# Kernel tuning notes

Hardware: AMD Instinct MI355X
Metric: run time of the kernel (lower is better)

The kernel has to match this reference:

```python
import jax, jax.numpy as jnp
import numpy as np
from jax import lax

# dims: S=seq_len, B=batch, D=word dim, HE=encoder hidden, HD=decoder hidden,
# E=atomic embedding dim, A=num_atomic, T=max_steps, SOS=start token id
S, B, D = 48, 64, 300
HE, HD, E, A, T, SOS = 300, 256, 50, 128, 50, 1


def _u(key, shape, scale):
    return jax.random.uniform(key, shape, jnp.float32, -scale, scale)


def setup_inputs() -> dict:
    key = jax.random.key(0)
    ks = iter(jax.random.split(key, 64))
    inp = {"word_vectors": jax.random.normal(next(ks), (S, B, D), jnp.float32)}
    se = 1.0 / np.sqrt(HE)
    for l, din in ((0, D), (1, 2 * HE)):
        for d in ("f", "b"):
            inp[f"e{l}{d}_Wih"] = _u(next(ks), (3 * HE, din), se)
            inp[f"e{l}{d}_Whh"] = _u(next(ks), (3 * HE, HE), se)
            inp[f"e{l}{d}_bih"] = _u(next(ks), (3 * HE,), se)
            inp[f"e{l}{d}_bhh"] = _u(next(ks), (3 * HE,), se)
    sd = 1.0 / np.sqrt(HD)
    for l, din in ((0, E), (1, HD)):
        inp[f"d{l}_Wih"] = _u(next(ks), (3 * HD, din), sd)
        inp[f"d{l}_Whh"] = _u(next(ks), (3 * HD, HD), sd)
        inp[f"d{l}_bih"] = _u(next(ks), (3 * HD,), sd)
        inp[f"d{l}_bhh"] = _u(next(ks), (3 * HD,), sd)
    emb = jax.random.normal(next(ks), (A, E), jnp.float32)
    inp["emb"] = emb.at[0].set(0.0)  # padding_idx=0
    inp["Wout"] = _u(next(ks), (A, HD), sd)
    inp["bout"] = _u(next(ks), (A,), sd)
    so = 1.0 / np.sqrt(D)
    inp["Wh0"] = _u(next(ks), (2 * HD, D), so)
    inp["bh0"] = _u(next(ks), (2 * HD,), so)
    return inp


def gru_cell(x, h, Wih, Whh, bih, bhh):
    # PyTorch GRU cell semantics
    gi = x @ Wih.T + bih
    gh = h @ Whh.T + bhh
    ir, iz, inn = jnp.split(gi, 3, axis=-1)
    hr, hz, hn = jnp.split(gh, 3, axis=-1)
    r = jax.nn.sigmoid(ir + hr)
    z = jax.nn.sigmoid(iz + hz)
    n = jnp.tanh(inn + r * hn)
    return (1.0 - z) * n + z * h


def gru_layer(xs, Wih, Whh, bih, bhh, reverse=False):
    # xs: [S, B, din] -> [S, B, H]; h0 = zeros (torch default)
    h0 = jnp.zeros((xs.shape[1], Whh.shape[1]), xs.dtype)
    def step(h, x):
        hn = gru_cell(x, h, Wih, Whh, bih, bhh)
        return hn, hn
    _, ys = lax.scan(step, h0, xs, reverse=reverse)
    return ys


def reference(word_vectors, e0f_Wih, e0f_Whh, e0f_bih, e0f_bhh, e0b_Wih, e0b_Whh, e0b_bih, e0b_bhh, e1f_Wih, e1f_Whh, e1f_bih, e1f_bhh, e1b_Wih, e1b_Whh, e1b_bih, e1b_bhh, d0_Wih, d0_Whh, d0_bih, d0_bhh, d1_Wih, d1_Whh, d1_bih, d1_bhh, emb, Wout, bout, Wh0, bh0):
    # --- encoder: 2-layer bidirectional GRU (eval mode: no dropout) ---
    x0f = gru_layer(word_vectors, e0f_Wih, e0f_Whh, e0f_bih, e0f_bhh, reverse=False)
    x0b = gru_layer(word_vectors, e0b_Wih, e0b_Whh, e0b_bih, e0b_bhh, reverse=True)
    x0 = jnp.concatenate([x0f, x0b], axis=-1)  # [S,B,2*HE]
    x1f = gru_layer(x0, e1f_Wih, e1f_Whh, e1f_bih, e1f_bhh, reverse=False)
    x1b = gru_layer(x0, e1b_Wih, e1b_Whh, e1b_bih, e1b_bhh, reverse=True)
    enc = x1f + x1b  # view(S,B,2,HE).sum(dim=2) of concat == sum of directions

    N = S * B
    h = jnp.tanh(enc @ Wh0.T + bh0).reshape(N, 2, HD)  # [N,2,HD]
    h0, h1 = h[:, 0], h[:, 1]
    e = jnp.broadcast_to(emb[SOS], (N, E))

    def step(carry, _):
        h0, h1, e = carry
        h0n = gru_cell(e, h0, d0_Wih, d0_Whh, d0_bih, d0_bhh)
        h1n = gru_cell(h0n, h1, d1_Wih, d1_Whh, d1_bih, d1_bhh)
        y = jax.nn.log_softmax(h1n @ Wout.T + bout, axis=-1)  # [N,A]
        p = jnp.argmax(y, axis=-1)
        return (h0n, h1n, emb[p]), y

    _, Y = lax.scan(step, (h0, h1, e), None, length=T)  # [T,N,A]
    return Y.reshape(T, S, B, A)[:-1]
```

## Files before the change

### kernel.cpp

```cpp
#include <hip/hip_runtime.h>
#include <math.h>

#define S_ 48
#define B_ 64
#define D_ 300
#define HE_ 300
#define HD_ 256
#define E_ 50
#define A_ 128
#define T_ 50
#define N_ (S_*B_)

__device__ __forceinline__ float sigm(float x){ return 1.0f/(1.0f + expf(-x)); }

template<int MODE>
__global__ __launch_bounds__(256)
void gemm_bias_kernel(const float* __restrict__ A, const float* __restrict__ A2,
                      const float* __restrict__ W,
                      const float* __restrict__ bias, float* __restrict__ C,
                      float* __restrict__ C2, int M, int N, int K)
{
  __shared__ float As[16][64];
  __shared__ float Ws[16][64];
  const int tid = threadIdx.x;
  const int bm = blockIdx.y * 64;
  const int bn = blockIdx.x * 64;
  const int tx = tid & 15, ty = tid >> 4;
  const int lr = tid >> 2;
  const int lk = (tid & 3) << 2;
  float acc[4][4] = {{0.f}};
  for (int kb = 0; kb < K; kb += 16) {
    {
      const int row = bm + lr;
      const int k = kb + lk;
      const float* ap = A + (size_t)row * K + k;
      float4 v = make_float4(0.f,0.f,0.f,0.f);
      if (k + 3 < K) v = *reinterpret_cast<const float4*>(ap);
      else {
        if (k   < K) v.x = ap[0];
        if (k+1 < K) v.y = ap[1];
        if (k+2 < K) v.z = ap[2];
        if (k+3 < K) v.w = ap[3];
      }
      if (MODE == 2) {
        const float* ap2 = A2 + (size_t)row * K + k;
        if (k + 3 < K) {
          float4 v2 = *reinterpret_cast<const float4*>(ap2);
          v.x += v2.x; v.y += v2.y; v.z += v2.z; v.w += v2.w;
        } else {
          if (k   < K) v.x += ap2[0];
          if (k+1 < K) v.y += ap2[1];
          if (k+2 < K) v.z += ap2[2];
          if (k+3 < K) v.w += ap2[3];
        }
      }
      As[lk][lr]=v.x; As[lk+1][lr]=v.y; As[lk+2][lr]=v.z; As[lk+3][lr]=v.w;
    }
    {
      const int col = bn + lr;
      const int k = kb + lk;
      float4 v = make_float4(0.f,0.f,0.f,0.f);
      if (col < N) {
        const float* wp = W + (size_t)col * K + k;
        if (k + 3 < K) v = *reinterpret_cast<const float4*>(wp);
        else {
          if (k   < K) v.x = wp[0];
          if (k+1 < K) v.y = wp[1];
          if (k+2 < K) v.z = wp[2];
          if (k+3 < K) v.w = wp[3];
        }
      }
      Ws[lk][lr]=v.x; Ws[lk+1][lr]=v.y; Ws[lk+2][lr]=v.z; Ws[lk+3][lr]=v.w;
    }
    __syncthreads();
    #pragma unroll
    for (int kk = 0; kk < 16; ++kk) {
      float4 a4 = *reinterpret_cast<const float4*>(&As[kk][ty<<2]);
      float4 w4 = *reinterpret_cast<const float4*>(&Ws[kk][tx<<2]);
      const float* a = reinterpret_cast<const float*>(&a4);
      const float* w = reinterpret_cast<const float*>(&w4);
      #pragma unroll
      for (int i = 0; i < 4; ++i)
        #pragma unroll
        for (int j = 0; j < 4; ++j)
          acc[i][j] = fmaf(a[i], w[j], acc[i][j]);
    }
    __syncthreads();
  }
  #pragma unroll
  for (int i = 0; i < 4; ++i) {
    const int m = bm + (ty<<2) + i;
    #pragma unroll
    for (int j = 0; j < 4; ++j) {
      const int n = bn + (tx<<2) + j;
      if (n < N) {
        float v = acc[i][j] + bias[n];
        if (MODE == 0) {
          C[(size_t)m*N + n] = v;
        } else {
          v = tanhf(v);
          if (n < HD_) C[(size_t)m*HD_ + n] = v;
          else         C2[(size_t)m*HD_ + (n-HD_)] = v;
        }
      }
    }
  }
}

__global__ __launch_bounds__(256)
void ctranspose_kernel(const float* __restrict__ in, float* __restrict__ out,
                       int NC, int NK, int NKP, int dstride, int row0, int coff)
{
  int idx = blockIdx.x * 256 + threadIdx.x;
  if (idx < NC*NKP) {
    int gc = idx / NKP, k = idx % NKP;
    out[(size_t)(row0+k)*dstride + coff + gc] =
        (k < NK) ? in[(size_t)gc*NK + k] : 0.0f;
  }
}

__global__ __launch_bounds__(256)
void pack4_kernel(const float* __restrict__ W, float4* __restrict__ P,
                  int NC, int NK, int K4)
{
  int idx = blockIdx.x * 256 + threadIdx.x;
  if (idx >= NC * K4) return;
  int k4 = idx / NC, gc = idx % NC;
  int k = k4 << 2;
  const float* wp = W + (size_t)gc * NK + k;
  float4 v = make_float4(0.f,0.f,0.f,0.f);
  if (k   < NK) v.x = wp[0];
  if (k+1 < NK) v.y = wp[1];
  if (k+2 < NK) v.z = wp[2];
  if (k+3 < NK) v.w = wp[3];
  P[(size_t)k4 * NC + gc] = v;
}

template<int LAYER>
__global__ __launch_bounds__(640, 2)
void enc_layer_persistent(const float* __restrict__ gi_f, const float* __restrict__ gi_b,
                          const float* __restrict__ WhhT_f, const float* __restrict__ WhhT_b,
                          const float* __restrict__ bhh_f, const float* __restrict__ bhh_b,
                          float* __restrict__ out, float* __restrict__ outB)
{
  const int dir = blockIdx.y;
  const float* gi  = dir ? gi_b   : gi_f;
  const float* WT  = dir ? WhhT_b : WhhT_f;
  const float* bhh = dir ? bhh_b  : bhh_f;
  float* o = (LAYER == 1 && dir) ? outB : out;

  __shared__ float hA[4][304];
  __shared__ float hB[4][304];
  const int tid = threadIdx.x;
  const int half = tid / 320;
  const int j = tid - half*320;
  const int R0 = blockIdx.x * 4;
  const int r0 = half * 2;
  const bool act = (j < HE_);

  float b_r = 0.f, b_z = 0.f, b_n = 0.f;
  if (act) { b_r = bhh[j]; b_z = bhh[HE_+j]; b_n = bhh[2*HE_+j]; }
  __syncthreads();

  for (int t = 0; t < S_; ++t) {
    const int tt = dir ? (S_-1 - t) : t;
    float (*hin)[304]  = (t & 1) ? hB : hA;
    float (*hout)[304] = (t & 1) ? hA : hB;
    float ar[2]={0,0}, az[2]={0,0}, an[2]={0,0};
    if (act && t > 0) {
      for (int k = 0; k < HE_; k += 4) {
        float wr[4], wz[4], wn[4];
        #pragma unroll
        for (int u = 0; u < 4; ++u) {
          const float* wk = WT + (size_t)(k+u)*(3*HE_);
          wr[u] = wk[j]; wz[u] = wk[HE_+j]; wn[u] = wk[2*HE_+j];
        }
        #pragma unroll
        for (int r = 0; r < 2; ++r) {
          float4 h4 = *reinterpret_cast<const float4*>(&hin[r0+r][k]);
          ar[r]=fmaf(h4.x,wr[0],ar[r]); ar[r]=fmaf(h4.y,wr[1],ar[r]);
          ar[r]=fmaf(h4.z,wr[2],ar[r]); ar[r]=fmaf(h4.w,wr[3],ar[r]);
          az[r]=fmaf(h4.x,wz[0],az[r]); az[r]=fmaf(h4.y,wz[1],az[r]);
          az[r]=fmaf(h4.z,wz[2],az[r]); az[r]=fmaf(h4.w,wz[3],az[r]);
          an[r]=fmaf(h4.x,wn[0],an[r]); an[r]=fmaf(h4.y,wn[1],an[r]);
          an[r]=fmaf(h4.z,wn[2],an[r]); an[r]=fmaf(h4.w,wn[3],an[r]);
        }
      }
    }
    if (act) {
      #pragma unroll
      for (int r = 0; r < 2; ++r) {
        const int row = R0 + r0 + r;
        const size_t gb = (size_t)(tt*B_ + row) * (3*HE_);
        float gr = gi[gb + j];
        float gz = gi[gb + HE_ + j];
        float gn = gi[gb + 2*HE_ + j];
        float rg = sigm(gr + ar[r] + b_r);
        float zg = sigm(gz + az[r] + b_z);
        float ng = tanhf(gn + rg*(an[r] + b_n));
        float ho = (t > 0) ? hin[r0+r][j] : 0.0f;
        float hn = (1.0f - zg)*ng + zg*ho;
        hout[r0+r][j] = hn;
        if (LAYER == 0) o[(size_t)(tt*B_ + row)*(2*HE_) + dir*HE_ + j] = hn;
        else            o[(size_t)(tt*B_ + row)*HE_ + j] = hn;
      }
    }
    __syncthreads();
  }
}

__global__ __launch_bounds__(512, 2)
void dec_persistent(const float4* __restrict__ Wih0P,
                    const float4* __restrict__ Whh0P,
                    const float4* __restrict__ Wih1P,
                    const float4* __restrict__ Whh1P,
                    const float* __restrict__ WoutT,
                    const float* __restrict__ bih0, const float* __restrict__ bhh0,
                    const float* __restrict__ bih1, const float* __restrict__ bhh1,
                    const float* __restrict__ bout,
                    const float* __restrict__ emb,
                    const float* __restrict__ h0init, const float* __restrict__ h1init,
                    float* __restrict__ Y)
{
  __shared__ __align__(16) float h0s[12][256];
  __shared__ __align__(16) float h1s[12][256];
  __shared__ __align__(16) float es[12][52];
  const int tid = threadIdx.x;
  const int R0 = blockIdx.x * 12;
  const int c  = tid & 255;
  const int half = tid >> 8;
  const int r0 = half * 6;
  const int lane = tid & 63;
  const int wave = tid >> 6;

  for (int i = tid; i < 12*64; i += 512) {
    int r = i >> 6, k = (i & 63) << 2;
    *reinterpret_cast<float4*>(&h0s[r][k]) =
        *reinterpret_cast<const float4*>(&h0init[(size_t)(R0+r)*HD_ + k]);
    *reinterpret_cast<float4*>(&h1s[r][k]) =
        *reinterpret_cast<const float4*>(&h1init[(size_t)(R0+r)*HD_ + k]);
  }
  for (int i = tid; i < 12*52; i += 512) {
    int r = i / 52, k = i - r*52;
    es[r][k] = (k < E_) ? emb[E_ + k] : 0.0f;
  }
  const float b0r = bih0[c] + bhh0[c];
  const float b0z = bih0[HD_+c] + bhh0[HD_+c];
  const float b0ni = bih0[2*HD_+c];
  const float b0nh = bhh0[2*HD_+c];
  const float b1r = bih1[c] + bhh1[c];
  const float b1z = bih1[HD_+c] + bhh1[HD_+c];
  const float b1ni = bih1[2*HD_+c];
  const float b1nh = bhh1[2*HD_+c];
  const float bo0 = bout[lane];
  const float bo1 = bout[64 + lane];
  __syncthreads();

  for (int s = 0; s < T_-1; ++s) {
    float ar[6]={0,0,0,0,0,0}, az[6]={0,0,0,0,0,0};
    float ani[6]={0,0,0,0,0,0}, anh[6]={0,0,0,0,0,0};
    for (int kq = 0; kq < 64; ++kq) {
      const int k = kq << 2;
      float4 wr = Whh0P[kq*768 + c];
      float4 wz = Whh0P[kq*768 + 256 + c];
      float4 wn = Whh0P[kq*768 + 512 + c];
      #pragma unroll
      for (int r = 0; r < 6; ++r) {
        float4 x = *reinterpret_cast<const float4*>(&h0s[r0+r][k]);
        ar[r]=fmaf(x.x,wr.x,ar[r]); ar[r]=fmaf(x.y,wr.y,ar[r]);
        ar[r]=fmaf(x.z,wr.z,ar[r]); ar[r]=fmaf(x.w,wr.w,ar[r]);
        az[r]=fmaf(x.x,wz.x,az[r]); az[r]=fmaf(x.y,wz.y,az[r]);
        az[r]=fmaf(x.z,wz.z,az[r]); az[r]=fmaf(x.w,wz.w,az[r]);
        anh[r]=fmaf(x.x,wn.x,anh[r]); anh[r]=fmaf(x.y,wn.y,anh[r]);
        anh[r]=fmaf(x.z,wn.z,anh[r]); anh[r]=fmaf(x.w,wn.w,anh[r]);
      }
      if (kq < 13) {
        float4 vr = Wih0P[kq*768 + c];
        float4 vz = Wih0P[kq*768 + 256 + c];
        float4 vn = Wih0P[kq*768 + 512 + c];
        #pragma unroll
        for (int r = 0; r < 6; ++r) {
          float4 e = *reinterpret_cast<const float4*>(&es[r0+r][k]);
          ar[r]=fmaf(e.x,vr.x,ar[r]); ar[r]=fmaf(e.y,vr.y,ar[r]);
          ar[r]=fmaf(e.z,vr.z,ar[r]); ar[r]=fmaf(e.w,vr.w,ar[r]);
          az[r]=fmaf(e.x,vz.x,az[r]); az[r]=fmaf(e.y,vz.y,az[r]);
          az[r]=fmaf(e.z,vz.z,az[r]); az[r]=fmaf(e.w,vz.w,az[r]);
          ani[r]=fmaf(e.x,vn.x,ani[r]); ani[r]=fmaf(e.y,vn.y,ani[r]);
          ani[r]=fmaf(e.z,vn.z,ani[r]); ani[r]=fmaf(e.w,vn.w,ani[r]);
        }
      }
    }
    __syncthreads();
    {
      float hnew[6];
      #pragma unroll
      for (int r = 0; r < 6; ++r) {
        float rg = sigm(ar[r] + b0r);
        float zg = sigm(az[r] + b0z);
        float ng = tanhf(ani[r] + b0ni + rg*(anh[r] + b0nh));
        float hold = h0s[r0+r][c];
        hnew[r] = (1.0f - zg)*ng + zg*hold;
      }
      #pragma unroll
      for (int r = 0; r < 6; ++r) h0s[r0+r][c] = hnew[r];
    }
    __syncthreads();
    #pragma unroll
    for (int r = 0; r < 6; ++r) { ar[r]=0.f; az[r]=0.f; ani[r]=0.f; anh[r]=0.f; }
    for (int kq = 0; kq < 64; ++kq) {
      const int k = kq << 2;
      float4 vr = Wih1P[kq*768 + c];
      float4 vz = Wih1P[kq*768 + 256 + c];
      float4 vn = Wih1P[kq*768 + 512 + c];
      float4 wr = Whh1P[kq*768 + c];
      float4 wz = Whh1P[kq*768 + 256 + c];
      float4 wn = Whh1P[kq*768 + 512 + c];
      #pragma unroll
      for (int r = 0; r < 6; ++r) {
        float4 x = *reinterpret_cast<const float4*>(&h0s[r0+r][k]);
        ar[r]=fmaf(x.x,vr.x,ar[r]); ar[r]=fmaf(x.y,vr.y,ar[r]);
        ar[r]=fmaf(x.z,vr.z,ar[r]); ar[r]=fmaf(x.w,vr.w,ar[r]);
        az[r]=fmaf(x.x,vz.x,az[r]); az[r]=fmaf(x.y,vz.y,az[r]);
        az[r]=fmaf(x.z,vz.z,az[r]); az[r]=fmaf(x.w,vz.w,az[r]);
        ani[r]=fmaf(x.x,vn.x,ani[r]); ani[r]=fmaf(x.y,vn.y,ani[r]);
        ani[r]=fmaf(x.z,vn.z,ani[r]); ani[r]=fmaf(x.w,vn.w,ani[r]);
        float4 y = *reinterpret_cast<const float4*>(&h1s[r0+r][k]);
        ar[r]=fmaf(y.x,wr.x,ar[r]); ar[r]=fmaf(y.y,wr.y,ar[r]);
        ar[r]=fmaf(y.z,wr.z,ar[r]); ar[r]=fmaf(y.w,wr.w,ar[r]);
        az[r]=fmaf(y.x,wz.x,az[r]); az[r]=fmaf(y.y,wz.y,az[r]);
        az[r]=fmaf(y.z,wz.z,az[r]); az[r]=fmaf(y.w,wz.w,az[r]);
        anh[r]=fmaf(y.x,wn.x,anh[r]); anh[r]=fmaf(y.y,wn.y,anh[r]);
        anh[r]=fmaf(y.z,wn.z,anh[r]); anh[r]=fmaf(y.w,wn.w,anh[r]);
      }
    }
    __syncthreads();
    {
      float hnew[6];
      #pragma unroll
      for (int r = 0; r < 6; ++r) {
        float rg = sigm(ar[r] + b1r);
        float zg = sigm(az[r] + b1z);
        float ng = tanhf(ani[r] + b1ni + rg*(anh[r] + b1nh));
        float hold = h1s[r0+r][c];
        hnew[r] = (1.0f - zg)*ng + zg*hold;
      }
      #pragma unroll
      for (int r = 0; r < 6; ++r) h1s[r0+r][c] = hnew[r];
    }
    __syncthreads();
    for (int rr = wave; rr < 12; rr += 8) {
      float a0 = 0.f, a1 = 0.f;
      for (int k = 0; k < HD_; k += 2) {
        float w00 = WoutT[(size_t)k*A_ + lane];
        float w01 = WoutT[(size_t)k*A_ + 64 + lane];
        float w10 = WoutT[(size_t)(k+1)*A_ + lane];
        float w11 = WoutT[(size_t)(k+1)*A_ + 64 + lane];
        float2 hv = *reinterpret_cast<const float2*>(&h1s[rr][k]);
        a0 = fmaf(hv.x, w00, a0); a0 = fmaf(hv.y, w10, a0);
        a1 = fmaf(hv.x, w01, a1); a1 = fmaf(hv.y, w11, a1);
      }
      float v0 = a0 + bo0;
      float v1 = a1 + bo1;
      float mx = fmaxf(v0, v1);
      #pragma unroll
      for (int off = 32; off >= 1; off >>= 1) mx = fmaxf(mx, __shfl_xor(mx, off));
      float sum = expf(v0 - mx) + expf(v1 - mx);
      #pragma unroll
      for (int off = 32; off >= 1; off >>= 1) sum += __shfl_xor(sum, off);
      float lz = mx + logf(sum);
      float* Yr = Y + ((size_t)s*N_ + R0 + rr)*A_;
      Yr[lane]      = v0 - lz;
      Yr[64 + lane] = v1 - lz;
      float bv; int bi;
      if (v0 >= v1) { bv = v0; bi = lane; } else { bv = v1; bi = 64 + lane; }
      #pragma unroll
      for (int off = 32; off >= 1; off >>= 1) {
        float ov = __shfl_xor(bv, off);
        int   oi = __shfl_xor(bi, off);
        if (ov > bv || (ov == bv && oi < bi)) { bv = ov; bi = oi; }
      }
      if (lane < E_) es[rr][lane] = emb[(size_t)bi*E_ + lane];
    }
    __syncthreads();
  }
}

extern "C" void kernel_launch(void* const* d_in, const int* in_sizes, int n_in,
                              void* d_out, int out_size, void* d_ws, size_t ws_size,
                              hipStream_t stream)
{
  (void)in_sizes; (void)n_in; (void)out_size; (void)ws_size;
  const float* wv      = (const float*)d_in[0];
  const float* e0f_Wih = (const float*)d_in[1];
  const float* e0f_Whh = (const float*)d_in[2];
  const float* e0f_bih = (const float*)d_in[3];
  const float* e0f_bhh = (const float*)d_in[4];
  const float* e0b_Wih = (const float*)d_in[5];
  const float* e0b_Whh = (const float*)d_in[6];
  const float* e0b_bih = (const float*)d_in[7];
  const float* e0b_bhh = (const float*)d_in[8];
  const float* e1f_Wih = (const float*)d_in[9];
  const float* e1f_Whh = (const float*)d_in[10];
  const float* e1f_bih = (const float*)d_in[11];
  const float* e1f_bhh = (const float*)d_in[12];
  const float* e1b_Wih = (const float*)d_in[13];
  const float* e1b_Whh = (const float*)d_in[14];
  const float* e1b_bih = (const float*)d_in[15];
  const float* e1b_bhh = (const float*)d_in[16];
  const float* d0_Wih  = (const float*)d_in[17];
  const float* d0_Whh  = (const float*)d_in[18];
  const float* d0_bih  = (const float*)d_in[19];
  const float* d0_bhh  = (const float*)d_in[20];
  const float* d1_Wih  = (const float*)d_in[21];
  const float* d1_Whh  = (const float*)d_in[22];
  const float* d1_bih  = (const float*)d_in[23];
  const float* d1_bhh  = (const float*)d_in[24];
  const float* emb     = (const float*)d_in[25];
  const float* Wout    = (const float*)d_in[26];
  const float* bout    = (const float*)d_in[27];
  const float* Wh0     = (const float*)d_in[28];
  const float* bh0     = (const float*)d_in[29];

  float* ws = (float*)d_ws;
  float* giA  = ws;
  float* giB  = giA + (size_t)N_*3*HE_;
  float* x0   = giB + (size_t)N_*3*HE_;
  float* eWhT = x0  + (size_t)N_*2*HE_;
  float* eT0f = eWhT;
  float* eT0b = eT0f + (size_t)3*HE_*HE_;
  float* eT1f = eT0b + (size_t)3*HE_*HE_;
  float* eT1b = eT1f + (size_t)3*HE_*HE_;
  float* encF = x0;
  float* encB = x0 + (size_t)N_*HE_;
  float* h0A  = giA;
  float* h1A  = giA + (size_t)N_*HD_;
  float4* Wih0P = (float4*)eWhT;
  float4* Whh0P = Wih0P + (size_t)13*768;
  float4* Wih1P = Whh0P + (size_t)64*768;
  float4* Whh1P = Wih1P + (size_t)64*768;
  float*  WoutT = (float*)(Whh1P + (size_t)64*768);
  float* Y = (float*)d_out;

  const dim3 blk(256);

  ctranspose_kernel<<<dim3(1055), blk, 0, stream>>>(e0f_Whh, eT0f, 3*HE_, HE_, HE_, 3*HE_, 0, 0);
  ctranspose_kernel<<<dim3(1055), blk, 0, stream>>>(e0b_Whh, eT0b, 3*HE_, HE_, HE_, 3*HE_, 0, 0);
  ctranspose_kernel<<<dim3(1055), blk, 0, stream>>>(e1f_Whh, eT1f, 3*HE_, HE_, HE_, 3*HE_, 0, 0);
  ctranspose_kernel<<<dim3(1055), blk, 0, stream>>>(e1b_Whh, eT1b, 3*HE_, HE_, HE_, 3*HE_, 0, 0);
  gemm_bias_kernel<0><<<dim3(15,48), blk, 0, stream>>>(wv, nullptr, e0f_Wih, e0f_bih, giA, nullptr, N_, 3*HE_, D_);
  gemm_bias_kernel<0><<<dim3(15,48), blk, 0, stream>>>(wv, nullptr, e0b_Wih, e0b_bih, giB, nullptr, N_, 3*HE_, D_);
  enc_layer_persistent<0><<<dim3(16,2), dim3(640), 0, stream>>>(giA, giB, eT0f, eT0b, e0f_bhh, e0b_bhh, x0, nullptr);
  gemm_bias_kernel<0><<<dim3(15,48), blk, 0, stream>>>(x0, nullptr, e1f_Wih, e1f_bih, giA, nullptr, N_, 3*HE_, 2*HE_);
  gemm_bias_kernel<0><<<dim3(15,48), blk, 0, stream>>>(x0, nullptr, e1b_Wih, e1b_bih, giB, nullptr, N_, 3*HE_, 2*HE_);
  enc_layer_persistent<1><<<dim3(16,2), dim3(640), 0, stream>>>(giA, giB, eT1f, eT1b, e1f_bhh, e1b_bhh, encF, encB);
  pack4_kernel<<<dim3(39),  blk, 0, stream>>>(d0_Wih, Wih0P, 3*HD_, E_,  13);
  pack4_kernel<<<dim3(192), blk, 0, stream>>>(d0_Whh, Whh0P, 3*HD_, HD_, 64);
  pack4_kernel<<<dim3(192), blk, 0, stream>>>(d1_Wih, Wih1P, 3*HD_, HD_, 64);
  pack4_kernel<<<dim3(192), blk, 0, stream>>>(d1_Whh, Whh1P, 3*HD_, HD_, 64);
  ctranspose_kernel<<<dim3(128), blk, 0, stream>>>(Wout, WoutT, A_, HD_, HD_, 128, 0, 0);
  gemm_bias_kernel<2><<<dim3(8,48), blk, 0, stream>>>(encF, encB, Wh0, bh0, h0A, h1A, N_, 2*HD_, HE_);
  dec_persistent<<<dim3(N_/12), dim3(512), 0, stream>>>(
      Wih0P, Whh0P, Wih1P, Whh1P, WoutT,
      d0_bih, d0_bhh, d1_bih, d1_bhh, bout,
      emb, h0A, h1A, Y);
}
```

Baseline: 7.015 ms.

## Split decoder gate columns across 768 threads, sharing r/z gates via LDS

```diff
diff --git a/kernel.cpp b/kernel.cpp
--- a/kernel.cpp
+++ b/kernel.cpp
@@ -209,7 +209,7 @@
   }
 }
 
-__global__ __launch_bounds__(512, 2)
+__global__ __launch_bounds__(768)
 void dec_persistent(const float4* __restrict__ Wih0P,
                     const float4* __restrict__ Whh0P,
                     const float4* __restrict__ Wih1P,
@@ -224,24 +224,26 @@
 {
   __shared__ __align__(16) float h0s[12][256];
   __shared__ __align__(16) float h1s[12][256];
-  __shared__ __align__(16) float es[12][52];
+  __shared__ __align__(16) float es[12][56];
+  __shared__ float grs[12][256];
+  __shared__ float gzs[12][256];
   const int tid = threadIdx.x;
   const int R0 = blockIdx.x * 12;
+  const int g  = tid;
   const int c  = tid & 255;
-  const int half = tid >> 8;
-  const int r0 = half * 6;
+  const int gt = tid >> 8;
   const int lane = tid & 63;
   const int wave = tid >> 6;
 
-  for (int i = tid; i < 12*64; i += 512) {
+  for (int i = tid; i < 12*64; i += 768) {
     int r = i >> 6, k = (i & 63) << 2;
     *reinterpret_cast<float4*>(&h0s[r][k]) =
         *reinterpret_cast<const float4*>(&h0init[(size_t)(R0+r)*HD_ + k]);
     *reinterpret_cast<float4*>(&h1s[r][k]) =
         *reinterpret_cast<const float4*>(&h1init[(size_t)(R0+r)*HD_ + k]);
   }
-  for (int i = tid; i < 12*52; i += 512) {
-    int r = i / 52, k = i - r*52;
+  for (int i = tid; i < 12*56; i += 768) {
+    int r = i / 56, k = i - r*56;
     es[r][k] = (k < E_) ? emb[E_ + k] : 0.0f;
   }
   const float b0r = bih0[c] + bhh0[c];
@@ -257,98 +259,130 @@
   __syncthreads();
 
   for (int s = 0; s < T_-1; ++s) {
-    float ar[6]={0,0,0,0,0,0}, az[6]={0,0,0,0,0,0};
-    float ani[6]={0,0,0,0,0,0}, anh[6]={0,0,0,0,0,0};
-    for (int kq = 0; kq < 64; ++kq) {
-      const int k = kq << 2;
-      float4 wr = Whh0P[kq*768 + c];
-      float4 wz = Whh0P[kq*768 + 256 + c];
-      float4 wn = Whh0P[kq*768 + 512 + c];
-      #pragma unroll
-      for (int r = 0; r < 6; ++r) {
-        float4 x = *reinterpret_cast<const float4*>(&h0s[r0+r][k]);
-        ar[r]=fmaf(x.x,wr.x,ar[r]); ar[r]=fmaf(x.y,wr.y,ar[r]);
-        ar[r]=fmaf(x.z,wr.z,ar[r]); ar[r]=fmaf(x.w,wr.w,ar[r]);
-        az[r]=fmaf(x.x,wz.x,az[r]); az[r]=fmaf(x.y,wz.y,az[r]);
-        az[r]=fmaf(x.z,wz.z,az[r]); az[r]=fmaf(x.w,wz.w,az[r]);
-        anh[r]=fmaf(x.x,wn.x,anh[r]); anh[r]=fmaf(x.y,wn.y,anh[r]);
-        anh[r]=fmaf(x.z,wn.z,anh[r]); anh[r]=fmaf(x.w,wn.w,anh[r]);
-      }
-      if (kq < 13) {
-        float4 vr = Wih0P[kq*768 + c];
-        float4 vz = Wih0P[kq*768 + 256 + c];
-        float4 vn = Wih0P[kq*768 + 512 + c];
-        #pragma unroll
-        for (int r = 0; r < 6; ++r) {
-          float4 e = *reinterpret_cast<const float4*>(&es[r0+r][k]);
-          ar[r]=fmaf(e.x,vr.x,ar[r]); ar[r]=fmaf(e.y,vr.y,ar[r]);
-          ar[r]=fmaf(e.z,vr.z,ar[r]); ar[r]=fmaf(e.w,vr.w,ar[r]);
-          az[r]=fmaf(e.x,vz.x,az[r]); az[r]=fmaf(e.y,vz.y,az[r]);
-          az[r]=fmaf(e.z,vz.z,az[r]); az[r]=fmaf(e.w,vz.w,az[r]);
-          ani[r]=fmaf(e.x,vn.x,ani[r]); ani[r]=fmaf(e.y,vn.y,ani[r]);
-          ani[r]=fmaf(e.z,vn.z,ani[r]); ani[r]=fmaf(e.w,vn.w,ani[r]);
-        }
-      }
-    }
-    __syncthreads();
+    if (gt < 2) {
+      float acc[12];
+      #pragma unroll
+      for (int r = 0; r < 12; ++r) acc[r] = 0.f;
+      for (int kq = 0; kq < 64; ++kq) {
+        const int k = kq << 2;
+        float4 w = Whh0P[kq*768 + g];
+        #pragma unroll
+        for (int r = 0; r < 12; ++r) {
+          float4 x = *reinterpret_cast<const float4*>(&h0s[r][k]);
+          acc[r]=fmaf(x.x,w.x,acc[r]); acc[r]=fmaf(x.y,w.y,acc[r]);
+          acc[r]=fmaf(x.z,w.z,acc[r]); acc[r]=fmaf(x.w,w.w,acc[r]);
+        }
+        if (kq < 13) {
+          float4 v = Wih0P[kq*768 + g];
+          #pragma unroll
+          for (int r = 0; r < 12; ++r) {
+            float4 e = *reinterpret_cast<const float4*>(&es[r][k]);
+            acc[r]=fmaf(e.x,v.x,acc[r]); acc[r]=fmaf(e.y,v.y,acc[r]);
+            acc[r]=fmaf(e.z,v.z,acc[r]); acc[r]=fmaf(e.w,v.w,acc[r]);
+          }
+        }
+      }
+      if (gt == 0) {
+        #pragma unroll
+        for (int r = 0; r < 12; ++r) grs[r][c] = acc[r];
+      } else {
+        #pragma unroll
+        for (int r = 0; r < 12; ++r) gzs[r][c] = acc[r];
+      }
+      __syncthreads();
+      __syncthreads();
+    } else {
+      float ani[12], anh[12];
+      #pragma unroll
+      for (int r = 0; r < 12; ++r) { ani[r] = 0.f; anh[r] = 0.f; }
+      for (int kq = 0; kq < 64; ++kq) {
+        const int k = kq << 2;
+        float4 w = Whh0P[kq*768 + g];
+        #pragma unroll
+        for (int r = 0; r < 12; ++r) {
+          float4 x = *reinterpret_cast<const float4*>(&h0s[r][k]);
+          anh[r]=fmaf(x.x,w.x,anh[r]); anh[r]=fmaf(x.y,w.y,anh[r]);
+          anh[r]=fmaf(x.z,w.z,anh[r]); anh[r]=fmaf(x.w,w.w,anh[r]);
+        }
+        if (kq < 13) {
+          float4 v = Wih0P[kq*768 + g];
+          #pragma unroll
+          for (int r = 0; r < 12; ++r) {
+            float4 e = *reinterpret_cast<const float4*>(&es[r][k]);
+            ani[r]=fmaf(e.x,v.x,ani[r]); ani[r]=fmaf(e.y,v.y,ani[r]);
+            ani[r]=fmaf(e.z,v.z,ani[r]); ani[r]=fmaf(e.w,v.w,ani[r]);
+          }
+        }
+      }
+      __syncthreads();
+      #pragma unroll
+      for (int r = 0; r < 12; ++r) {
+        float rg = sigm(grs[r][c] + b0r);
+        float zg = sigm(gzs[r][c] + b0z);
+        float ng = tanhf(ani[r] + b0ni + rg*(anh[r] + b0nh));
+        float hold = h0s[r][c];
+        h0s[r][c] = (1.0f - zg)*ng + zg*hold;
+      }
+      __syncthreads();
+    }
+    if (gt < 2) {
+      float acc[12];
+      #pragma unroll
+      for (int r = 0; r < 12; ++r) acc[r] = 0.f;
+      for (int kq = 0; kq < 64; ++kq) {
+        const int k = kq << 2;
+        float4 v = Wih1P[kq*768 + g];
+        float4 w = Whh1P[kq*768 + g];
+        #pragma unroll
+        for (int r = 0; r < 12; ++r) {
+          float4 x = *reinterpret_cast<const float4*>(&h0s[r][k]);
+          acc[r]=fmaf(x.x,v.x,acc[r]); acc[r]=fmaf(x.y,v.y,acc[r]);
+          acc[r]=fmaf(x.z,v.z,acc[r]); acc[r]=fmaf(x.w,v.w,acc[r]);
+          float4 y = *reinterpret_cast<const float4*>(&h1s[r][k]);
+          acc[r]=fmaf(y.x,w.x,acc[r]); acc[r]=fmaf(y.y,w.y,acc[r]);
+          acc[r]=fmaf(y.z,w.z,acc[r]); acc[r]=fmaf(y.w,w.w,acc[r]);
+        }
+      }
+      if (gt == 0) {
+        #pragma unroll
+        for (int r = 0; r < 12; ++r) grs[r][c] = acc[r];
+      } else {
+        #pragma unroll
+        for (int r = 0; r < 12; ++r) gzs[r][c] = acc[r];
+      }
+      __syncthreads();
+      __syncthreads();
+    } else {
+      float ani[12], anh[12];
+      #pragma unroll
+      for (int r = 0; r < 12; ++r) { ani[r] = 0.f; anh[r] = 0.f; }
+      for (int kq = 0; kq < 64; ++kq) {
+        const int k = kq << 2;
+        float4 v = Wih1P[kq*768 + g];
+        float4 w = Whh1P[kq*768 + g];
+        #pragma unroll
+        for (int r = 0; r < 12; ++r) {
+          float4 x = *reinterpret_cast<const float4*>(&h0s[r][k]);
+          ani[r]=fmaf(x.x,v.x,ani[r]); ani[r]=fmaf(x.y,v.y,ani[r]);
+          ani[r]=fmaf(x.z,v.z,ani[r]); ani[r]=fmaf(x.w,v.w,ani[r]);
+          float4 y = *reinterpret_cast<const float4*>(&h1s[r][k]);
+          anh[r]=fmaf(y.x,w.x,anh[r]); anh[r]=fmaf(y.y,w.y,anh[r]);
+          anh[r]=fmaf(y.z,w.z,anh[r]); anh[r]=fmaf(y.w,w.w,anh[r]);
+        }
+      }
+      __syncthreads();
+      #pragma unroll
+      for (int r = 0; r < 12; ++r) {
+        float rg = sigm(grs[r][c] + b1r);
+        float zg = sigm(gzs[r][c] + b1z);
+        float ng = tanhf(ani[r] + b1ni + rg*(anh[r] + b1nh));
+        float hold = h1s[r][c];
+        h1s[r][c] = (1.0f - zg)*ng + zg*hold;
+      }
+      __syncthreads();
+    }
     {
-      float hnew[6];
-      #pragma unroll
-      for (int r = 0; r < 6; ++r) {
-        float rg = sigm(ar[r] + b0r);
-        float zg = sigm(az[r] + b0z);
-        float ng = tanhf(ani[r] + b0ni + rg*(anh[r] + b0nh));
-        float hold = h0s[r0+r][c];
-        hnew[r] = (1.0f - zg)*ng + zg*hold;
-      }
-      #pragma unroll
-      for (int r = 0; r < 6; ++r) h0s[r0+r][c] = hnew[r];
-    }
-    __syncthreads();
-    #pragma unroll
-    for (int r = 0; r < 6; ++r) { ar[r]=0.f; az[r]=0.f; ani[r]=0.f; anh[r]=0.f; }
-    for (int kq = 0; kq < 64; ++kq) {
-      const int k = kq << 2;
-      float4 vr = Wih1P[kq*768 + c];
-      float4 vz = Wih1P[kq*768 + 256 + c];
-      float4 vn = Wih1P[kq*768 + 512 + c];
-      float4 wr = Whh1P[kq*768 + c];
-      float4 wz = Whh1P[kq*768 + 256 + c];
-      float4 wn = Whh1P[kq*768 + 512 + c];
-      #pragma unroll
-      for (int r = 0; r < 6; ++r) {
-        float4 x = *reinterpret_cast<const float4*>(&h0s[r0+r][k]);
-        ar[r]=fmaf(x.x,vr.x,ar[r]); ar[r]=fmaf(x.y,vr.y,ar[r]);
-        ar[r]=fmaf(x.z,vr.z,ar[r]); ar[r]=fmaf(x.w,vr.w,ar[r]);
-        az[r]=fmaf(x.x,vz.x,az[r]); az[r]=fmaf(x.y,vz.y,az[r]);
-        az[r]=fmaf(x.z,vz.z,az[r]); az[r]=fmaf(x.w,vz.w,az[r]);
-        ani[r]=fmaf(x.x,vn.x,ani[r]); ani[r]=fmaf(x.y,vn.y,ani[r]);
-        ani[r]=fmaf(x.z,vn.z,ani[r]); ani[r]=fmaf(x.w,vn.w,ani[r]);
-        float4 y = *reinterpret_cast<const float4*>(&h1s[r0+r][k]);
-        ar[r]=fmaf(y.x,wr.x,ar[r]); ar[r]=fmaf(y.y,wr.y,ar[r]);
-        ar[r]=fmaf(y.z,wr.z,ar[r]); ar[r]=fmaf(y.w,wr.w,ar[r]);
-        az[r]=fmaf(y.x,wz.x,az[r]); az[r]=fmaf(y.y,wz.y,az[r]);
-        az[r]=fmaf(y.z,wz.z,az[r]); az[r]=fmaf(y.w,wz.w,az[r]);
-        anh[r]=fmaf(y.x,wn.x,anh[r]); anh[r]=fmaf(y.y,wn.y,anh[r]);
-        anh[r]=fmaf(y.z,wn.z,anh[r]); anh[r]=fmaf(y.w,wn.w,anh[r]);
-      }
-    }
-    __syncthreads();
-    {
-      float hnew[6];
-      #pragma unroll
-      for (int r = 0; r < 6; ++r) {
-        float rg = sigm(ar[r] + b1r);
-        float zg = sigm(az[r] + b1z);
-        float ng = tanhf(ani[r] + b1ni + rg*(anh[r] + b1nh));
-        float hold = h1s[r0+r][c];
-        hnew[r] = (1.0f - zg)*ng + zg*hold;
-      }
-      #pragma unroll
-      for (int r = 0; r < 6; ++r) h1s[r0+r][c] = hnew[r];
-    }
-    __syncthreads();
-    for (int rr = wave; rr < 12; rr += 8) {
+      const int rr = wave;
       float a0 = 0.f, a1 = 0.f;
       for (int k = 0; k < HD_; k += 2) {
         float w00 = WoutT[(size_t)k*A_ + lane];
@@ -459,7 +493,7 @@
   pack4_kernel<<<dim3(192), blk, 0, stream>>>(d1_Whh, Whh1P, 3*HD_, HD_, 64);
   ctranspose_kernel<<<dim3(128), blk, 0, stream>>>(Wout, WoutT, A_, HD_, HD_, 128, 0, 0);
   gemm_bias_kernel<2><<<dim3(8,48), blk, 0, stream>>>(encF, encB, Wh0, bh0, h0A, h1A, N_, 2*HD_, HE_);
-  dec_persistent<<<dim3(N_/12), dim3(512), 0, stream>>>(
+  dec_persistent<<<dim3(N_/12), dim3(768), 0, stream>>>(
       Wih0P, Whh0P, Wih1P, Whh1P, WoutT,
       d0_bih, d0_bhh, d1_bih, d1_bhh, bout,
       emb, h0A, h1A, Y);
```

Measured after the change: 7.902 ms. 1.13x slower.
